# Optimization experiments

Hardware: AMD Instinct MI355X
Metric: run time of the kernel (lower is better)

Reference implementation:

```python
import jax, jax.numpy as jnp
import numpy as np

B, T, E = 2, 2048, 1024   # batch, block_size, emb_d
H, D = 16, 64             # heads, head_size


def setup_inputs() -> dict:
    key = jax.random.key(0)
    ks = jax.random.split(key, 7)
    s = 1.0 / np.sqrt(E)
    inputs = jax.random.normal(ks[0], (B, T, E), dtype=jnp.float32)
    k_w = jax.random.uniform(ks[1], (H, E, D), jnp.float32, -s, s)
    k_b = jax.random.uniform(ks[2], (H, D), jnp.float32, -s, s)
    q_w = jax.random.uniform(ks[3], (H, E, D), jnp.float32, -s, s)
    q_b = jax.random.uniform(ks[4], (H, D), jnp.float32, -s, s)
    v_w = jax.random.uniform(ks[5], (H, E, D), jnp.float32, -s, s)
    v_b = jax.random.uniform(ks[6], (H, D), jnp.float32, -s, s)
    return {"inputs": inputs, "k_w": k_w, "k_b": k_b,
            "q_w": q_w, "q_b": q_b, "v_w": v_w, "v_b": v_b}


def reference(inputs, k_w, k_b, q_w, q_b, v_w, v_b):
    # Per-head linear projections, vectorized over heads: (B,T,E)x(H,E,D)->(B,H,T,D)
    k = jnp.einsum('bte,hed->bhtd', inputs, k_w) + k_b[None, :, None, :]
    q = jnp.einsum('bte,hed->bhtd', inputs, q_w) + q_b[None, :, None, :]
    v = jnp.einsum('bte,hed->bhtd', inputs, v_w) + v_b[None, :, None, :]

    scale = D ** (-0.5)
    # scores: (B,H,Tq,Tk)
    w = jnp.einsum('bhtd,bhsd->bhts', q, k) * scale
    tril = jnp.tril(jnp.ones((T, T), dtype=bool))
    w = jnp.where(tril[None, None, :, :], w, -jnp.inf)
    # NOTE: original torch code does softmax(weights, dim=1) on a (B,T,T)
    # tensor, i.e. over the QUERY axis. Faithfully reproduce: axis=-2 here.
    w = jax.nn.softmax(w, axis=-2)
    out = jnp.einsum('bhts,bhsd->bhtd', w, v)           # (B,H,T,D)
    # concat heads along last dim, head-major order matching torch.cat
    return out.transpose(0, 2, 1, 3).reshape(B, T, H * D)
```

## Files before the change

### kernel.cpp

```cpp
#include <hip/hip_runtime.h>
#include <hip/hip_bf16.h>
#include <math.h>

#define B_ 2
#define T_ 2048
#define E_ 1024
#define H_ 16
#define D_ 64
#define NT_ 32
#define QSCALE 0.180336880f

typedef __attribute__((ext_vector_type(8))) short bf16x8;
typedef __attribute__((ext_vector_type(4))) float f32x4;

#if __has_builtin(__builtin_amdgcn_exp2f)
#define EXP2(x) __builtin_amdgcn_exp2f(x)
#else
#define EXP2(x) exp2f(x)
#endif

__device__ __forceinline__ unsigned short f2bf(float x) {
  union { float f; unsigned u; } v; v.f = x;
  unsigned r = v.u + 0x7FFFu + ((v.u >> 16) & 1u);
  return (unsigned short)(r >> 16);
}
__device__ __forceinline__ unsigned pk2bf(float a, float b) {
  __hip_bfloat162 h = __float22bfloat162_rn(make_float2(a, b));
  union { __hip_bfloat162 h; unsigned u; } c; c.h = h; return c.u;
}

__device__ __forceinline__ void dma8(const unsigned short* g, int gstride,
                                     unsigned short* l, int lane)
{
  const int r = lane >> 3, bg = (lane & 7) ^ (r & 7);
  __builtin_amdgcn_global_load_lds(
      (const __attribute__((address_space(1))) void*)(g + (size_t)r * gstride + bg * 8),
      (__attribute__((address_space(3))) void*)l, 16, 0, 0);
}
__device__ __forceinline__ bf16x8 frag(const unsigned short* tile, int row, int g) {
  return *(const bf16x8*)(tile + row * 64 + (((g ^ row) & 7) << 3));
}

__global__ __launch_bounds__(256) void pack_kernel(
    const float* __restrict__ in, unsigned short* __restrict__ o16,
    const float* __restrict__ qw, const float* __restrict__ kw, const float* __restrict__ vw,
    unsigned short* __restrict__ qwt, unsigned short* __restrict__ kwt,
    unsigned short* __restrict__ vwt)
{
  __shared__ float s[64][65];
  const int tid = threadIdx.x;
  if (blockIdx.x < 2048) {
    const size_t i = ((size_t)blockIdx.x * 256 + tid) * 8;
    float4 f0 = *(const float4*)(in + i);
    float4 f1 = *(const float4*)(in + i + 4);
    unsigned u[4] = { pk2bf(f0.x, f0.y), pk2bf(f0.z, f0.w),
                      pk2bf(f1.x, f1.y), pk2bf(f1.z, f1.w) };
    *(bf16x8*)(o16 + i) = *(const bf16x8*)u;
    return;
  }
  const int i = blockIdx.x - 2048;
  const int e0 = (i & 15) * 64, h = (i >> 4) & 15, z = i >> 8;
  const float* w = (z == 0) ? qw : (z == 1) ? kw : vw;
  unsigned short* o = (z == 0) ? qwt : (z == 1) ? kwt : vwt;
  {
    const int r = tid >> 2;
    #pragma unroll
    for (int p = 0; p < 4; ++p) {
      const int c = (tid & 3) * 4 + p * 16;
      float4 f = *(const float4*)(w + ((size_t)(h * E_ + e0 + r)) * D_ + c);
      s[r][c] = f.x; s[r][c+1] = f.y; s[r][c+2] = f.z; s[r][c+3] = f.w;
    }
  }
  __syncthreads();
  {
    const int d = tid >> 2, ec = (tid & 3) * 16;
    unsigned short tmp[16];
    #pragma unroll
    for (int j = 0; j < 16; ++j) tmp[j] = f2bf(s[ec + j][d]);
    unsigned short* dst = o + ((size_t)(h * D_ + d)) * E_ + e0 + ec;
    *(bf16x8*)(dst)     = *(const bf16x8*)&tmp[0];
    *(bf16x8*)(dst + 8) = *(const bf16x8*)&tmp[8];
  }
}

__global__ __launch_bounds__(256) void proj_kernel(
    const unsigned short* __restrict__ in16,
    const unsigned short* __restrict__ qwt, const unsigned short* __restrict__ kwt,
    const unsigned short* __restrict__ vwt,
    const float* __restrict__ qb, const float* __restrict__ kb, const float* __restrict__ vb,
    unsigned short* __restrict__ qo, unsigned short* __restrict__ ko,
    unsigned short* __restrict__ vt)
{
  __shared__ __align__(16) unsigned short in_s[2][128 * 64];
  __shared__ __align__(16) unsigned short w_s[2][3 * 64 * 64];
  const int tid = threadIdx.x;
  const int lane = tid & 63, wv = tid >> 6;
  const int l15 = lane & 15, quad = lane >> 4;
  const int lin = blockIdx.x;
  const int h = ((lin & 7) << 1) | ((lin >> 3) & 1);
  const int rem = lin >> 4;
  const int t0 = (rem & 15) * 128, b = rem >> 4;
  const int bh = b * H_ + h;
  const unsigned short* wts[3] = { qwt, kwt, vwt };

  f32x4 acc[3][8];
  #pragma unroll
  for (int x = 0; x < 3; ++x)
    #pragma unroll
    for (int tb = 0; tb < 8; ++tb) acc[x][tb] = (f32x4){0.f, 0.f, 0.f, 0.f};

#define PROJ_STAGE(e0_, bi_)                                                      \
  {                                                                               \
    const unsigned short* gin = in16 + ((size_t)(b * T_ + t0)) * E_ + (e0_);      \
    _Pragma("unroll")                                                             \
    for (int p = 0; p < 4; ++p) {                                                 \
      const int br = wv * 32 + p * 8;                                             \
      dma8(gin + (size_t)br * E_, E_, &in_s[bi_][br * 64], lane);                 \
    }                                                                             \
    _Pragma("unroll")                                                             \
    for (int j = 0; j < 6; ++j) {                                                 \
      const int idx = wv * 6 + j;                                                 \
      const int x = idx >> 3, br = (idx & 7) * 8;                                 \
      dma8(wts[x] + ((size_t)(h * D_ + br)) * E_ + (e0_), E_,                     \
           &w_s[bi_][x * 4096 + br * 64], lane);                                  \
    }                                                                             \
  }

  PROJ_STAGE(0, 0);
  __syncthreads();
  for (int e = 0; e < 16; ++e) {
    const int bi = e & 1;
    if (e < 15) PROJ_STAGE((e + 1) * 64, bi ^ 1);
    const unsigned short* is = in_s[bi];
    const unsigned short* ws = w_s[bi];
    #pragma unroll
    for (int kk = 0; kk < 2; ++kk) {
      const int g0 = kk * 4 + quad;
      bf16x8 bfr[3];
      #pragma unroll
      for (int x = 0; x < 3; ++x)
        bfr[x] = frag(ws, x * 64 + wv * 16 + l15, g0);
      bf16x8 afr[8];
      #pragma unroll
      for (int tb = 0; tb < 8; ++tb)
        afr[tb] = frag(is, tb * 16 + l15, g0);
      #pragma unroll
      for (int tb = 0; tb < 8; ++tb) {
        acc[0][tb] = __builtin_amdgcn_mfma_f32_16x16x32_bf16(bfr[0], afr[tb], acc[0][tb], 0, 0, 0);
        acc[1][tb] = __builtin_amdgcn_mfma_f32_16x16x32_bf16(bfr[1], afr[tb], acc[1][tb], 0, 0, 0);
        acc[2][tb] = __builtin_amdgcn_mfma_f32_16x16x32_bf16(afr[tb], bfr[2], acc[2][tb], 0, 0, 0);
      }
    }
    __syncthreads();
  }
#undef PROJ_STAGE

  const size_t obase = (size_t)bh * T_;
  #pragma unroll
  for (int x = 0; x < 2; ++x) {
    const float scl = (x == 0) ? QSCALE : 1.0f;
    const float* bias = (x == 0) ? qb : kb;
    unsigned short* outp = (x == 0) ? qo : ko;
    float bias4[4];
    *(float4*)bias4 = *(const float4*)&bias[h * D_ + wv * 16 + quad * 4];
    #pragma unroll
    for (int tb = 0; tb < 8; ++tb) {
      const int t = t0 + tb * 16 + l15;
      unsigned short pk[4];
      #pragma unroll
      for (int r = 0; r < 4; ++r) pk[r] = f2bf((acc[x][tb][r] + bias4[r]) * scl);
      *(ushort4*)(outp + (obase + t) * D_ + wv * 16 + quad * 4) = *(const ushort4*)pk;
    }
  }
  {
    const int d = wv * 16 + l15;
    const float bvv = vb[h * D_ + d];
    #pragma unroll
    for (int tb = 0; tb < 8; ++tb) {
      const int t = t0 + tb * 16 + quad * 4;
      unsigned short pk[4];
      #pragma unroll
      for (int r = 0; r < 4; ++r) pk[r] = f2bf(acc[2][tb][r] + bvv);
      *(ushort4*)(vt + ((size_t)(bh * D_ + d)) * T_ + t) = *(const ushort4*)pk;
    }
  }
}

__global__ __launch_bounds__(256) void stats_kernel(
    const unsigned short* __restrict__ q, const unsigned short* __restrict__ k,
    float* __restrict__ lg)
{
  __shared__ __align__(16) unsigned short q_s[3][64 * 64];
  __shared__ float red[4][64];
  const int tid = threadIdx.x;
  const int lane = tid & 63, wv = tid >> 6;
  const int l15 = lane & 15, quad = lane >> 4;
  const int h = blockIdx.x, b = blockIdx.y, sa = blockIdx.z;
  const int bh = b * H_ + h;
  const int s0 = sa * 64;
  const unsigned short* qbase = q + (size_t)bh * T_ * 64;

  bf16x8 kf[4][2];
  #pragma unroll
  for (int nb = 0; nb < 4; ++nb)
    #pragma unroll
    for (int kk = 0; kk < 2; ++kk)
      kf[nb][kk] = *(const bf16x8*)(k + ((size_t)(bh * T_ + s0 + nb * 16 + l15)) * 64
                                      + kk * 32 + quad * 8);

#define ST_STAGE(tt_, slot_)                                                 \
  { _Pragma("unroll")                                                        \
    for (int pp = 0; pp < 2; ++pp) {                                         \
      const int br = wv * 16 + pp * 8;                                       \
      dma8(qbase + (size_t)((tt_) * 64 + br) * 64, 64, &q_s[slot_][br * 64], lane); \
    } }

  ST_STAGE(sa, 0);
  if (sa + 1 < NT_) ST_STAGE(sa + 1, 1);

  float lsum[4] = {0.f, 0.f, 0.f, 0.f};

  for (int tt = sa; tt < NT_; ++tt) {
    const int i = tt - sa;
    if (tt + 1 < NT_) asm volatile("s_waitcnt vmcnt(2)" ::: "memory");
    else              asm volatile("s_waitcnt vmcnt(0)" ::: "memory");
    __builtin_amdgcn_sched_barrier(0);

    const unsigned short* qs = q_s[i % 3];
    bf16x8 a0 = frag(qs, wv * 16 + l15, quad);
    bf16x8 a1 = frag(qs, wv * 16 + l15, 4 + quad);
    if (tt + 2 < NT_) ST_STAGE(tt + 2, (i + 2) % 3);

    f32x4 sacc[4];
    #pragma unroll
    for (int nb = 0; nb < 4; ++nb) sacc[nb] = (f32x4){0.f, 0.f, 0.f, 0.f};
    #pragma unroll
    for (int nb = 0; nb < 4; ++nb) {
      sacc[nb] = __builtin_amdgcn_mfma_f32_16x16x32_bf16(a0, kf[nb][0], sacc[nb], 0, 0, 0);
      sacc[nb] = __builtin_amdgcn_mfma_f32_16x16x32_bf16(a1, kf[nb][1], sacc[nb], 0, 0, 0);
    }
    if (tt == sa) {
      const int tbase = tt * 64 + wv * 16 + quad * 4;
      #pragma unroll
      for (int nb = 0; nb < 4; ++nb) {
        const int s = s0 + nb * 16 + l15;
        #pragma unroll
        for (int r = 0; r < 4; ++r)
          lsum[nb] += (tbase + r >= s) ? EXP2(sacc[nb][r]) : 0.f;
      }
    } else {
      #pragma unroll
      for (int nb = 0; nb < 4; ++nb)
        #pragma unroll
        for (int r = 0; r < 4; ++r) lsum[nb] += EXP2(sacc[nb][r]);
    }
  }
#undef ST_STAGE
  #pragma unroll
  for (int nb = 0; nb < 4; ++nb) {
    lsum[nb] += __shfl_xor(lsum[nb], 16);
    lsum[nb] += __shfl_xor(lsum[nb], 32);
  }
  if (lane < 16) {
    #pragma unroll
    for (int nb = 0; nb < 4; ++nb) red[wv][nb * 16 + lane] = lsum[nb];
  }
  __syncthreads();
  if (tid < 64) {
    const float L = red[0][tid] + red[1][tid] + red[2][tid] + red[3][tid];
    lg[(size_t)bh * T_ + s0 + tid] = -__log2f(L);
  }
}

__global__ __launch_bounds__(256) void out_kernel(
    const unsigned short* __restrict__ q, const unsigned short* __restrict__ k,
    const unsigned short* __restrict__ vt, const float* __restrict__ lg,
    float* __restrict__ out)
{
  __shared__ __align__(16) unsigned short k_s[2][64 * 64];
  __shared__ __align__(16) unsigned short vt_s[2][64 * 64];
  __shared__ __align__(16) unsigned short u_s[4][32][40];
  __shared__ float lg_sh[2][64];
  const int tid = threadIdx.x;
  const int lane = tid & 63, wv = tid >> 6;
  const int l15 = lane & 15, quad = lane >> 4;
  const int th = wv >> 1, sh = wv & 1;
  const int h = blockIdx.x, b = blockIdx.y, jt = 31 - blockIdx.z;
  const int bh = b * H_ + h;
  const int t0 = jt * 64;
  const unsigned short* kbase = k + (size_t)bh * T_ * 64;
  const unsigned short* vbase = vt + (size_t)bh * D_ * T_;
  const float* lgbase = lg + (size_t)bh * T_;

  bf16x8 qf[2][2];
  #pragma unroll
  for (int nt = 0; nt < 2; ++nt) {
    const unsigned short* qrow = q + (size_t)(bh * T_ + t0 + th * 32 + nt * 16 + l15) * 64;
    qf[nt][0] = *(const bf16x8*)(qrow + quad * 8);
    qf[nt][1] = *(const bf16x8*)(qrow + 32 + quad * 8);
  }

  #pragma unroll
  for (int pp = 0; pp < 2; ++pp) {
    const int br = wv * 16 + pp * 8;
    dma8(kbase + (size_t)br * 64, 64, &k_s[0][br * 64], lane);
    dma8(vbase + (size_t)br * T_, T_, &vt_s[0][br * 64], lane);
  }
  if (tid < 64) lg_sh[0][tid] = lgbase[tid];
  __syncthreads();

  f32x4 oacc[4][2];
  #pragma unroll
  for (int mb = 0; mb < 4; ++mb)
    #pragma unroll
    for (int nt = 0; nt < 2; ++nt) oacc[mb][nt] = (f32x4){0.f, 0.f, 0.f, 0.f};

  for (int st = 0; st <= jt; ++st) {
    const int bi = st & 1;
    if (st < jt) {
      const int s1 = (st + 1) * 64;
      #pragma unroll
      for (int pp = 0; pp < 2; ++pp) {
        const int br = wv * 16 + pp * 8;
        dma8(kbase + (size_t)(s1 + br) * 64, 64, &k_s[bi ^ 1][br * 64], lane);
        dma8(vbase + (size_t)br * T_ + s1, T_, &vt_s[bi ^ 1][br * 64], lane);
      }
      if (tid < 64) lg_sh[bi ^ 1][tid] = lgbase[s1 + tid];
    }
    const unsigned short* ks = k_s[bi];
    const unsigned short* vs = vt_s[bi];
    const float* lgb = lg_sh[bi];

    const bool dead = (st == jt) && (th == 0) && (sh == 1);
    if (!dead) {
      f32x4 sacc[2][2];
      #pragma unroll
      for (int mb = 0; mb < 2; ++mb) {
        float lg4[4];
        *(float4*)lg4 = *(const float4*)&lgb[sh * 32 + mb * 16 + quad * 4];
        #pragma unroll
        for (int nt = 0; nt < 2; ++nt)
          sacc[mb][nt] = (f32x4){lg4[0], lg4[1], lg4[2], lg4[3]};
      }
      #pragma unroll
      for (int mb = 0; mb < 2; ++mb) {
        bf16x8 ka0 = frag(ks, sh * 32 + mb * 16 + l15, quad);
        bf16x8 ka1 = frag(ks, sh * 32 + mb * 16 + l15, 4 + quad);
        #pragma unroll
        for (int nt = 0; nt < 2; ++nt) {
          sacc[mb][nt] = __builtin_amdgcn_mfma_f32_16x16x32_bf16(ka0, qf[nt][0], sacc[mb][nt], 0, 0, 0);
          sacc[mb][nt] = __builtin_amdgcn_mfma_f32_16x16x32_bf16(ka1, qf[nt][1], sacc[mb][nt], 0, 0, 0);
        }
      }
      const bool diagmask = (st == jt) && (th == sh);
      #pragma unroll
      for (int mb = 0; mb < 2; ++mb)
        #pragma unroll
        for (int nt = 0; nt < 2; ++nt) {
          float uu[4] = { EXP2(sacc[mb][nt][0]), EXP2(sacc[mb][nt][1]),
                          EXP2(sacc[mb][nt][2]), EXP2(sacc[mb][nt][3]) };
          if (diagmask) {
            const int tl = nt * 16 + l15, sl = mb * 16 + quad * 4;
            #pragma unroll
            for (int r = 0; r < 4; ++r) if (tl < sl + r) uu[r] = 0.f;
          }
          *(uint2*)(&u_s[wv][nt * 16 + l15][mb * 16 + quad * 4]) =
              make_uint2(pk2bf(uu[0], uu[1]), pk2bf(uu[2], uu[3]));
        }
      #pragma unroll
      for (int nt = 0; nt < 2; ++nt) {
        bf16x8 ua = *(const bf16x8*)(&u_s[wv][nt * 16 + l15][quad * 8]);
        #pragma unroll
        for (int mb = 0; mb < 4; ++mb)
          oacc[mb][nt] = __builtin_amdgcn_mfma_f32_16x16x32_bf16(
              frag(vs, mb * 16 + l15, sh * 4 + quad), ua, oacc[mb][nt], 0, 0, 0);
      }
    }
    __syncthreads();
  }

  float* scr = (float*)k_s;
  if (sh == 1) {
    #pragma unroll
    for (int mb = 0; mb < 4; ++mb)
      #pragma unroll
      for (int nt = 0; nt < 2; ++nt) {
        float o4[4] = { oacc[mb][nt][0], oacc[mb][nt][1], oacc[mb][nt][2], oacc[mb][nt][3] };
        *(float4*)&scr[((th * 8 + mb * 2 + nt) * 64 + lane) * 4] = *(const float4*)o4;
      }
  }
  __syncthreads();
  if (sh == 0) {
    #pragma unroll
    for (int nt = 0; nt < 2; ++nt) {
      float* orow = out + ((size_t)(b * T_ + t0 + th * 32 + nt * 16 + l15)) * (H_ * D_) + h * D_;
      #pragma unroll
      for (int mb = 0; mb < 4; ++mb) {
        float4 p = *(const float4*)&scr[((th * 8 + mb * 2 + nt) * 64 + lane) * 4];
        float o4[4] = { oacc[mb][nt][0] + p.x, oacc[mb][nt][1] + p.y,
                        oacc[mb][nt][2] + p.z, oacc[mb][nt][3] + p.w };
        *(float4*)(orow + mb * 16 + quad * 4) = *(const float4*)o4;
      }
    }
  }
}

extern "C" void kernel_launch(void* const* d_in, const int* in_sizes, int n_in,
                              void* d_out, int out_size, void* d_ws, size_t ws_size,
                              hipStream_t stream) {
  const float* in = (const float*)d_in[0];
  const float* kw = (const float*)d_in[1];
  const float* kb = (const float*)d_in[2];
  const float* qw = (const float*)d_in[3];
  const float* qb = (const float*)d_in[4];
  const float* vw = (const float*)d_in[5];
  const float* vb = (const float*)d_in[6];
  float* out = (float*)d_out;

  unsigned short* p = (unsigned short*)d_ws;
  const size_t inz = (size_t)B_ * T_ * E_;
  const size_t wz  = (size_t)H_ * D_ * E_;
  const size_t qz  = (size_t)B_ * H_ * T_ * D_;
  unsigned short* in16 = p;            p += inz;
  unsigned short* qwt  = p;            p += wz;
  unsigned short* kwt  = p;            p += wz;
  unsigned short* vwt  = p;            p += wz;
  unsigned short* q16  = p;            p += qz;
  unsigned short* k16  = p;            p += qz;
  unsigned short* vtb  = p;            p += qz;
  float* lgbuf = (float*)p;

  dim3 blk(256);
  pack_kernel <<<dim3(2048 + 768), blk, 0, stream>>>(in, in16, qw, kw, vw, qwt, kwt, vwt);
  proj_kernel <<<dim3(512), blk, 0, stream>>>(in16, qwt, kwt, vwt,
                                              qb, kb, vb, q16, k16, vtb);
  stats_kernel<<<dim3(H_, B_, NT_), blk, 0, stream>>>(q16, k16, lgbuf);
  out_kernel  <<<dim3(H_, B_, NT_), blk, 0, stream>>>(q16, k16, vtb, lgbuf, out);
}
```

Measured before the change: 168.5 us.

## Widen out_kernel query tile to 128 rows with 512-thread blocks

```diff
diff --git a/kernel.cpp b/kernel.cpp
--- a/kernel.cpp
+++ b/kernel.cpp
@@ -272,22 +272,25 @@
   }
 }
 
-__global__ __launch_bounds__(256) void out_kernel(
+__global__ __launch_bounds__(512) void out_kernel(
     const unsigned short* __restrict__ q, const unsigned short* __restrict__ k,
     const unsigned short* __restrict__ vt, const float* __restrict__ lg,
     float* __restrict__ out)
 {
-  __shared__ __align__(16) unsigned short k_s[2][64 * 64];
-  __shared__ __align__(16) unsigned short vt_s[2][64 * 64];
-  __shared__ __align__(16) unsigned short u_s[4][32][40];
-  __shared__ float lg_sh[2][64];
+  __shared__ __align__(16) unsigned char smem[53760];
+  unsigned short (*k_s)[4096]   = (unsigned short (*)[4096])(smem);
+  unsigned short (*vt_s)[4096]  = (unsigned short (*)[4096])(smem + 16384);
+  unsigned short (*u_s)[32][40] = (unsigned short (*)[32][40])(smem + 32768);
+  float (*lg_sh)[64]            = (float (*)[64])(smem + 53248);
+
   const int tid = threadIdx.x;
   const int lane = tid & 63, wv = tid >> 6;
   const int l15 = lane & 15, quad = lane >> 4;
   const int th = wv >> 1, sh = wv & 1;
-  const int h = blockIdx.x, b = blockIdx.y, jt = 31 - blockIdx.z;
+  const int h = blockIdx.x, b = blockIdx.y, tb2 = 15 - blockIdx.z;
   const int bh = b * H_ + h;
-  const int t0 = jt * 64;
+  const int t0 = tb2 * 128;
+  const int smax = 2 * tb2 + 1;
   const unsigned short* kbase = k + (size_t)bh * T_ * 64;
   const unsigned short* vbase = vt + (size_t)bh * D_ * T_;
   const float* lgbase = lg + (size_t)bh * T_;
@@ -300,12 +303,12 @@
     qf[nt][1] = *(const bf16x8*)(qrow + 32 + quad * 8);
   }
 
-  #pragma unroll
-  for (int pp = 0; pp < 2; ++pp) {
-    const int br = wv * 16 + pp * 8;
-    dma8(kbase + (size_t)br * 64, 64, &k_s[0][br * 64], lane);
-    dma8(vbase + (size_t)br * T_, T_, &vt_s[0][br * 64], lane);
-  }
+#define OUT_STAGE(soff_, slot_)                                               \
+  { const int br = wv * 8;                                                    \
+    dma8(kbase + (size_t)((soff_) + br) * 64, 64, &k_s[slot_][br * 64], lane);\
+    dma8(vbase + (size_t)br * T_ + (soff_), T_, &vt_s[slot_][br * 64], lane); }
+
+  OUT_STAGE(0, 0);
   if (tid < 64) lg_sh[0][tid] = lgbase[tid];
   __syncthreads();
 
@@ -315,23 +318,22 @@
     #pragma unroll
     for (int nt = 0; nt < 2; ++nt) oacc[mb][nt] = (f32x4){0.f, 0.f, 0.f, 0.f};
 
-  for (int st = 0; st <= jt; ++st) {
+  const int tmin = t0 + th * 32;
+
+  for (int st = 0; st <= smax; ++st) {
     const int bi = st & 1;
-    if (st < jt) {
+    if (st < smax) {
       const int s1 = (st + 1) * 64;
-      #pragma unroll
-      for (int pp = 0; pp < 2; ++pp) {
-        const int br = wv * 16 + pp * 8;
-        dma8(kbase + (size_t)(s1 + br) * 64, 64, &k_s[bi ^ 1][br * 64], lane);
-        dma8(vbase + (size_t)br * T_ + s1, T_, &vt_s[bi ^ 1][br * 64], lane);
-      }
+      OUT_STAGE(s1, bi ^ 1);
       if (tid < 64) lg_sh[bi ^ 1][tid] = lgbase[s1 + tid];
     }
     const unsigned short* ks = k_s[bi];
     const unsigned short* vs = vt_s[bi];
     const float* lgb = lg_sh[bi];
 
-    const bool dead = (st == jt) && (th == 0) && (sh == 1);
+    const int smin = st * 64 + sh * 32;
+    const bool dead  = (tmin + 31) < smin;
+    const bool diagm = !dead && (tmin <= smin + 31);
     if (!dead) {
       f32x4 sacc[2][2];
       #pragma unroll
@@ -352,17 +354,17 @@
           sacc[mb][nt] = __builtin_amdgcn_mfma_f32_16x16x32_bf16(ka1, qf[nt][1], sacc[mb][nt], 0, 0, 0);
         }
       }
-      const bool diagmask = (st == jt) && (th == sh);
       #pragma unroll
       for (int mb = 0; mb < 2; ++mb)
         #pragma unroll
         for (int nt = 0; nt < 2; ++nt) {
           float uu[4] = { EXP2(sacc[mb][nt][0]), EXP2(sacc[mb][nt][1]),
                           EXP2(sacc[mb][nt][2]), EXP2(sacc[mb][nt][3]) };
-          if (diagmask) {
-            const int tl = nt * 16 + l15, sl = mb * 16 + quad * 4;
+          if (diagm) {
+            const int tg = tmin + nt * 16 + l15;
+            const int sg = smin + mb * 16 + quad * 4;
             #pragma unroll
-            for (int r = 0; r < 4; ++r) if (tl < sl + r) uu[r] = 0.f;
+            for (int r = 0; r < 4; ++r) if (tg < sg + r) uu[r] = 0.f;
           }
           *(uint2*)(&u_s[wv][nt * 16 + l15][mb * 16 + quad * 4]) =
               make_uint2(pk2bf(uu[0], uu[1]), pk2bf(uu[2], uu[3]));
@@ -378,8 +380,9 @@
     }
     __syncthreads();
   }
-
-  float* scr = (float*)k_s;
+#undef OUT_STAGE
+
+  float* scr = (float*)smem;
   if (sh == 1) {
     #pragma unroll
     for (int mb = 0; mb < 4; ++mb)
@@ -435,5 +438,5 @@
   proj_kernel <<<dim3(512), blk, 0, stream>>>(in16, qwt, kwt, vwt,
                                               qb, kb, vb, q16, k16, vtb);
   stats_kernel<<<dim3(H_, B_, NT_), blk, 0, stream>>>(q16, k16, lgbuf);
-  out_kernel  <<<dim3(H_, B_, NT_), blk, 0, stream>>>(q16, k16, vtb, lgbuf, out);
-}
+  out_kernel  <<<dim3(H_, B_, 16), dim3(512), 0, stream>>>(q16, k16, vtb, lgbuf, out);
+}
```

New measurement: 169.7 us. About the same (+0.7%).
